# Kernel optimization log

Hardware: AMD Instinct MI355X
Metric: run time of the kernel (lower is better)

The kernel has to match this reference:

```python
import jax, jax.numpy as jnp
import numpy as np


def setup_inputs() -> dict:
    key = jax.random.key(0)
    ks = jax.random.split(key, 7)
    S, B, I, H = 512, 64, 1024, 1024
    s = 1.0 / np.sqrt(H)  # torch Linear default init scale
    return {
        "x": jax.random.normal(ks[0], (S, B, I), dtype=jnp.float32),
        "h0": jax.random.normal(ks[1], (B, H), dtype=jnp.float32),
        "c0": jax.random.normal(ks[2], (B, H), dtype=jnp.float32),
        "W_ih": jax.random.normal(ks[3], (4 * H, I), dtype=jnp.float32) * s,
        "b_ih": jax.random.normal(ks[4], (4 * H,), dtype=jnp.float32) * s,
        "W_hh": jax.random.normal(ks[5], (4 * H, H), dtype=jnp.float32) * s,
        "b_hh": jax.random.normal(ks[6], (4 * H,), dtype=jnp.float32) * s,
    }


def reference(x, h0, c0, W_ih, b_ih, W_hh, b_hh):
    # x: [S, B, I]; LSTM scan over time. Precompute input projections in one
    # big GEMM (mathematically identical to per-step linear_ih).
    H = h0.shape[-1]
    gates_x = jnp.einsum('sbi,gi->sbg', x, W_ih) + b_ih + b_hh  # [S, B, 4H]

    def step(carry, gx):
        h, c = carry
        gates = gx + h @ W_hh.T  # [B, 4H]
        i_g, f_g, g_g, o_g = jnp.split(gates, 4, axis=-1)
        i_g = jax.nn.sigmoid(i_g)
        f_g = jax.nn.sigmoid(f_g)
        g_g = jnp.tanh(g_g)
        o_g = jax.nn.sigmoid(o_g)
        c_new = f_g * c + i_g * g_g
        h_new = o_g * jnp.tanh(c_new)
        return (h_new, c_new), h_new

    (h_last, c_last), output = jax.lax.scan(step, (h0, c0), gates_x)
    return output, (h_last, c_last)
```

## Files before the change

kernel.cpp:

```cpp
#include <hip/hip_runtime.h>
#include <hip/hip_bf16.h>
#include <math.h>


#define S_LEN 512
#define BATCH 64
#define IDIM 1024
#define HDIM 1024
#define GDIM 4096
#define MAGIC 0x1337BEEFu
#define HSLOT (BATCH * HDIM)
#define NRING 4
#define RB 16

typedef __bf16 bf16x8 __attribute__((ext_vector_type(8)));
typedef float f32x4 __attribute__((ext_vector_type(4)));

__device__ inline ushort f2b(float f) {
    union { float f; unsigned u; } v; v.f = f;
    unsigned u = v.u;
    unsigned r = (u + 0x7fffu + ((u >> 16) & 1u)) >> 16;
    return (ushort)r;
}
__device__ inline float b2f(ushort u) {
    union { unsigned u; float f; } v; v.u = ((unsigned)u) << 16;
    return v.f;
}
__device__ inline float sigmoidf_(float x) { return 1.f / (1.f + __expf(-x)); }
__device__ inline float tanhf_(float x) {
    return 1.f - 2.f / (__expf(2.f * x) + 1.f);
}

__global__ __launch_bounds__(256) void f2b_kernel(ushort* __restrict__ dst,
                                                  const float* __restrict__ src, int n) {
    int i = (blockIdx.x * 256 + threadIdx.x) * 4;
    if (i < n) {
        float4 v = *(const float4*)(src + i);
        ushort4 o;
        o.x = f2b(v.x); o.y = f2b(v.y); o.z = f2b(v.z); o.w = f2b(v.w);
        *(ushort4*)(dst + i) = o;
    }
}

__global__ __launch_bounds__(256) void bias_kernel(float* __restrict__ bias,
                                                   const float* __restrict__ b_ih,
                                                   const float* __restrict__ b_hh) {
    int i = blockIdx.x * 256 + threadIdx.x;
    if (i < GDIM) bias[i] = b_ih[i] + b_hh[i];
}

#define LDSS 72
__global__ __launch_bounds__(256) void gemm_bt_kernel(const ushort* __restrict__ A,
                                                      const ushort* __restrict__ B,
                                                      ushort* __restrict__ C,
                                                      int M, int N, int K) {
    __shared__ __align__(16) ushort As[128 * LDSS];
    __shared__ __align__(16) ushort Bs[128 * LDSS];
    const int tid = threadIdx.x;
    const int lane = tid & 63;
    const int wave = tid >> 6;
    const int l15 = lane & 15;
    const int quad = lane >> 4;
    const int bn = blockIdx.x;
    const int bm = blockIdx.y;
    const int wrow = (wave & 1) * 64;
    const int wcol = (wave >> 1) * 64;

    f32x4 acc[4][4] = {};

    for (int kt = 0; kt < K; kt += 64) {
        #pragma unroll
        for (int i = 0; i < 4; i++) {
            int chunk = tid + i * 256;
            int r = chunk >> 3;
            int c8 = (chunk & 7) * 8;
            *(uint4*)&As[r * LDSS + c8] =
                *(const uint4*)&A[(size_t)(bm * 128 + r) * K + kt + c8];
            *(uint4*)&Bs[r * LDSS + c8] =
                *(const uint4*)&B[(size_t)(bn * 128 + r) * K + kt + c8];
        }
        __syncthreads();
        #pragma unroll
        for (int kc = 0; kc < 2; kc++) {
            const int ko = kc * 32 + quad * 8;
            bf16x8 af[4], bf[4];
            #pragma unroll
            for (int m = 0; m < 4; m++)
                af[m] = *(const bf16x8*)&As[(wrow + m * 16 + l15) * LDSS + ko];
            #pragma unroll
            for (int n = 0; n < 4; n++)
                bf[n] = *(const bf16x8*)&Bs[(wcol + n * 16 + l15) * LDSS + ko];
            #pragma unroll
            for (int m = 0; m < 4; m++)
                #pragma unroll
                for (int n = 0; n < 4; n++)
                    acc[m][n] = __builtin_amdgcn_mfma_f32_16x16x32_bf16(af[m], bf[n], acc[m][n], 0, 0, 0);
        }
        __syncthreads();
    }
    const int col0 = bn * 128 + wcol;
    const int row0 = bm * 128 + wrow;
    #pragma unroll
    for (int m = 0; m < 4; m++) {
        #pragma unroll
        for (int n = 0; n < 4; n++) {
            int col = col0 + n * 16 + l15;
            int rbase = row0 + m * 16 + quad * 4;
            #pragma unroll
            for (int r = 0; r < 4; r++)
                C[(size_t)(rbase + r) * N + col] = f2b(acc[m][n][r]);
        }
    }
}

#define HS2 1032
#define GS_BS 17
#define GS_GATE (16 * GS_BS)
#define GS_KH (4 * GS_GATE)

__global__ __launch_bounds__(512, 2) void lstm_persistent(
    const ushort* __restrict__ gx,
    ushort* __restrict__ hring,
    const ushort* __restrict__ Whh,
    const float* __restrict__ bias,
    const float* __restrict__ c0,
    float* __restrict__ out,
    unsigned* __restrict__ flags)
{
    __shared__ __align__(16) ushort Hs[RB * HS2];
    __shared__ float Gs[2 * GS_KH];

    const int tid = threadIdx.x;
    const int lane = tid & 63;
    const int wv = tid >> 6;
    const int gate = wv & 3;
    const int kh = wv >> 2;
    const int l15 = lane & 15;
    const int quad = lane >> 4;
    const int bid = blockIdx.x;
    const int ring = bid >> 6;
    const int blk = bid & 63;

    bf16x8 wf[16];
    {
        const ushort* wrow = Whh + ((size_t)(gate * 1024 + blk * 16 + l15)) * 1024
                           + kh * 512 + quad * 8;
        #pragma unroll
        for (int ks = 0; ks < 16; ks++)
            wf[ks] = *(const bf16x8*)(wrow + ks * 32);
    }

    const bool pw = (tid < 128);
    const int pb = tid >> 3;
    const int pj = (tid * 2) & 15;
    const int gb = ring * RB + pb;
    const int pcol = blk * 16 + pj;
    float2 creg = {0.f, 0.f};
    if (pw) creg = *(const float2*)&c0[(size_t)gb * HDIM + pcol];
    float bsum[4][2];
    #pragma unroll
    for (int g = 0; g < 4; g++) {
        bsum[g][0] = bias[g * 1024 + pcol];
        bsum[g][1] = bias[g * 1024 + pcol + 1];
    }
    const size_t gx_tb = (size_t)gb * GDIM + blk * 16 + pj;

    #pragma unroll 1
    for (int s = 0; s < S_LEN; s++) {
        const ushort* hsrc = hring + (size_t)s * HSLOT + (size_t)ring * RB * HDIM;

        ushort2 gxr[4] = {};
        if (pw) {
            const ushort* gxs = gx + (size_t)s * BATCH * GDIM + gx_tb;
            #pragma unroll
            for (int g = 0; g < 4; g++)
                gxr[g] = *(const ushort2*)(gxs + g * 1024);
        }

        if (s > 0) {
            if (wv == 0) {
                const unsigned* fl = flags + ((size_t)s * NRING + ring) * 64;
                while (true) {
                    unsigned v = __hip_atomic_load(&fl[lane], __ATOMIC_RELAXED,
                                                   __HIP_MEMORY_SCOPE_AGENT);
                    if (__ballot(v != MAGIC) == 0ull) break;
                    __builtin_amdgcn_s_sleep(2);
                }
            }
            __syncthreads();
        }

        {
            const unsigned long long* h64 = (const unsigned long long*)hsrc;
            unsigned long long hr[8];
            #pragma unroll
            for (int c = 0; c < 8; c++)
                hr[c] = __hip_atomic_load(&h64[c * 512 + tid], __ATOMIC_RELAXED,
                                          __HIP_MEMORY_SCOPE_AGENT);
            #pragma unroll
            for (int c = 0; c < 8; c++) {
                int u = c * 512 + tid;
                int row = u >> 8;
                int col = (u & 255) * 4;
                *(unsigned long long*)&Hs[row * HS2 + col] = hr[c];
            }
        }
        __syncthreads();

        f32x4 acc = {0.f, 0.f, 0.f, 0.f};
        const int arow = l15 * HS2 + kh * 512 + quad * 8;
        #pragma unroll
        for (int ks = 0; ks < 16; ks++) {
            bf16x8 a = *(const bf16x8*)&Hs[arow + ks * 32];
            acc = __builtin_amdgcn_mfma_f32_16x16x32_bf16(a, wf[ks], acc, 0, 0, 0);
        }

        #pragma unroll
        for (int r = 0; r < 4; r++)
            Gs[kh * GS_KH + gate * GS_GATE + (quad * 4 + r) * GS_BS + l15] = acc[r];
        __syncthreads();

        float hv[2], cv[2];
        if (pw) {
            #pragma unroll
            for (int u = 0; u < 2; u++) {
                float cold = u ? creg.y : creg.x;
                int gsb = pb * GS_BS + pj + u;
                float g0 = Gs[0 * GS_GATE + gsb] + Gs[GS_KH + 0 * GS_GATE + gsb] + bsum[0][u] + b2f(u ? gxr[0].y : gxr[0].x);
                float g1 = Gs[1 * GS_GATE + gsb] + Gs[GS_KH + 1 * GS_GATE + gsb] + bsum[1][u] + b2f(u ? gxr[1].y : gxr[1].x);
                float g2 = Gs[2 * GS_GATE + gsb] + Gs[GS_KH + 2 * GS_GATE + gsb] + bsum[2][u] + b2f(u ? gxr[2].y : gxr[2].x);
                float g3 = Gs[3 * GS_GATE + gsb] + Gs[GS_KH + 3 * GS_GATE + gsb] + bsum[3][u] + b2f(u ? gxr[3].y : gxr[3].x);
                float ig = sigmoidf_(g0);
                float fg = sigmoidf_(g1);
                float gg = tanhf_(g2);
                float og = sigmoidf_(g3);
                float cn = fg * cold + ig * gg;
                float hn = og * tanhf_(cn);
                cv[u] = cn; hv[u] = hn;
            }
            creg.x = cv[0]; creg.y = cv[1];

            if (s < S_LEN - 1) {
                ushort* hdst = hring + (size_t)(s + 1) * HSLOT;
                unsigned hword = (unsigned)f2b(hv[0]) | ((unsigned)f2b(hv[1]) << 16);
                __hip_atomic_store((unsigned*)&hdst[(size_t)gb * HDIM + pcol], hword,
                                   __ATOMIC_RELAXED, __HIP_MEMORY_SCOPE_AGENT);
            }
        }

        __syncthreads();
        if (tid == 0 && s < S_LEN - 1) {
            asm volatile("s_waitcnt vmcnt(0)" ::: "memory");
            __hip_atomic_store(&flags[((size_t)(s + 1) * NRING + ring) * 64 + blk],
                               MAGIC, __ATOMIC_RELAXED, __HIP_MEMORY_SCOPE_AGENT);
        }

        if (pw) {
            float2 ho; ho.x = hv[0]; ho.y = hv[1];
            *(float2*)&out[(size_t)s * BATCH * HDIM + (size_t)gb * HDIM + pcol] = ho;
            if (s == S_LEN - 1) {
                float* tail = out + (size_t)S_LEN * BATCH * HDIM;
                *(float2*)&tail[(size_t)gb * HDIM + pcol] = ho;
                float2 co; co.x = cv[0]; co.y = cv[1];
                *(float2*)&tail[BATCH * HDIM + (size_t)gb * HDIM + pcol] = co;
            }
        }
    }
}

extern "C" void kernel_launch(void* const* d_in, const int* in_sizes, int n_in,
                              void* d_out, int out_size, void* d_ws, size_t ws_size,
                              hipStream_t stream) {
    const float* x    = (const float*)d_in[0];
    const float* h0   = (const float*)d_in[1];
    const float* c0   = (const float*)d_in[2];
    const float* W_ih = (const float*)d_in[3];
    const float* b_ih = (const float*)d_in[4];
    const float* W_hh = (const float*)d_in[5];
    const float* b_hh = (const float*)d_in[6];
    float* out = (float*)d_out;

    const size_t n_x  = (size_t)S_LEN * BATCH * IDIM;
    const size_t n_w  = (size_t)GDIM * IDIM;
    const size_t o_xb    = 0;
    const size_t o_gx    = o_xb + n_x * 2;
    const size_t o_wih   = o_gx + (size_t)S_LEN * BATCH * GDIM * 2;
    const size_t o_whh   = o_wih + n_w * 2;
    const size_t o_bias  = o_whh + n_w * 2;
    const size_t o_flags = o_bias + GDIM * 4;
    const size_t flags_bytes = (size_t)(S_LEN + 1) * NRING * 64 * 4;
    const size_t total  = o_flags + flags_bytes;
    if (ws_size < total) return;

    char* ws = (char*)d_ws;
    ushort* xb   = (ushort*)(ws + o_xb);
    ushort* hring = xb;
    ushort* gx   = (ushort*)(ws + o_gx);
    ushort* wihb = (ushort*)(ws + o_wih);
    ushort* whhb = (ushort*)(ws + o_whh);
    float*  bias = (float*)(ws + o_bias);
    unsigned* flags = (unsigned*)(ws + o_flags);

    f2b_kernel<<<(int)(n_x / 1024), 256, 0, stream>>>(xb, x, (int)n_x);
    f2b_kernel<<<(int)(n_w / 1024), 256, 0, stream>>>(wihb, W_ih, (int)n_w);
    f2b_kernel<<<(int)(n_w / 1024), 256, 0, stream>>>(whhb, W_hh, (int)n_w);
    bias_kernel<<<GDIM / 256, 256, 0, stream>>>(bias, b_ih, b_hh);
    hipMemsetAsync(flags, 0, flags_bytes, stream);

    {
        dim3 grid(GDIM / 128, (S_LEN * BATCH) / 128);
        gemm_bt_kernel<<<grid, 256, 0, stream>>>(xb, wihb, gx, S_LEN * BATCH, IDIM == 0 ? 0 : GDIM, IDIM);
    }

    f2b_kernel<<<(BATCH * HDIM) / 1024, 256, 0, stream>>>(hring, h0, BATCH * HDIM);

    {
        const ushort* gx_c = gx;
        const ushort* whh_c = whhb;
        const float* bias_c = bias;
        void* args[] = { (void*)&gx_c, (void*)&hring, (void*)&whh_c,
                         (void*)&bias_c, (void*)&c0, (void*)&out, (void*)&flags };
        hipLaunchCooperativeKernel((const void*)lstm_persistent, dim3(NRING * 64), dim3(512),
                                   args, 0, stream);
    }
}
```

Baseline: 2.328 ms.

## Pin LSTM batch rings to XCDs so sync stays in local L2

The persistent LSTM is repartitioned into 8 batch rings of 8 rows, with 32 blocks per ring each owning 32 hidden columns (two MFMA column groups). At startup each block reads its XCC_ID and claims a slot, so every ring lives entirely on one XCD. When that placement succeeds, flag polling, h writes and h reads use plain or workgroup-scope accesses that stay in the local L2 instead of agent-scope coherent traffic. The aim is to cut cross-XCD synchronisation latency per timestep. The cost is a startup grid barrier and a fallback path, and correctness relies on the assumption that same-XCD L2 coherence holds for these non-atomic accesses.

```diff
diff --git a/kernel.cpp b/kernel.cpp
--- a/kernel.cpp
+++ b/kernel.cpp
@@ -10,8 +10,10 @@
 #define GDIM 4096
 #define MAGIC 0x1337BEEFu
 #define HSLOT (BATCH * HDIM)
-#define NRING 4
-#define RB 16
+#define NRING 8
+#define RB 8
+#define NBLK 32
+#define CPB 32
 
 typedef __bf16 bf16x8 __attribute__((ext_vector_type(8)));
 typedef float f32x4 __attribute__((ext_vector_type(4)));
@@ -114,9 +116,7 @@
 }
 
 #define HS2 1032
-#define GS_BS 17
-#define GS_GATE (16 * GS_BS)
-#define GS_KH (4 * GS_GATE)
+#define GS_CS 33
 
 __global__ __launch_bounds__(512, 2) void lstm_persistent(
     const ushort* __restrict__ gx,
@@ -125,10 +125,12 @@
     const float* __restrict__ bias,
     const float* __restrict__ c0,
     float* __restrict__ out,
-    unsigned* __restrict__ flags)
+    unsigned* __restrict__ flags,
+    unsigned* __restrict__ claim)
 {
-    __shared__ __align__(16) ushort Hs[RB * HS2];
-    __shared__ float Gs[2 * GS_KH];
+    __shared__ __align__(16) ushort Hs[16 * HS2];
+    __shared__ float Gs[2 * 4 * 16 * GS_CS];
+    __shared__ int sh_ring, sh_pos, sh_ok;
 
     const int tid = threadIdx.x;
     const int lane = tid & 63;
@@ -138,23 +140,51 @@
     const int l15 = lane & 15;
     const int quad = lane >> 4;
     const int bid = blockIdx.x;
-    const int ring = bid >> 6;
-    const int blk = bid & 63;
-
-    bf16x8 wf[16];
+
+    if (tid == 0) {
+        unsigned xcd;
+        asm volatile("s_getreg_b32 %0, hwreg(HW_REG_XCC_ID)" : "=s"(xcd));
+        xcd &= 7;
+        int p = (int)__hip_atomic_fetch_add(&claim[xcd], 1u, __ATOMIC_RELAXED,
+                                            __HIP_MEMORY_SCOPE_AGENT);
+        __hip_atomic_fetch_add(&claim[8], 1u, __ATOMIC_RELEASE,
+                               __HIP_MEMORY_SCOPE_AGENT);
+        while (__hip_atomic_load(&claim[8], __ATOMIC_RELAXED,
+                                 __HIP_MEMORY_SCOPE_AGENT) < NRING * NBLK)
+            __builtin_amdgcn_s_sleep(8);
+        int ok = 1;
+        #pragma unroll
+        for (int i = 0; i < 8; i++)
+            ok &= (__hip_atomic_load(&claim[i], __ATOMIC_RELAXED,
+                                     __HIP_MEMORY_SCOPE_AGENT) == NBLK);
+        sh_ring = ok ? (int)xcd : (bid & 7);
+        sh_pos  = ok ? p : (bid >> 3);
+        sh_ok = ok;
+    }
+    for (int i = tid; i < 8 * HS2; i += 512) Hs[8 * HS2 + i] = 0;
+    __syncthreads();
+    const int ring = sh_ring;
+    const int pos = sh_pos;
+    const bool l2ok = (sh_ok != 0);
+
+    bf16x8 wf[2][16];
     {
-        const ushort* wrow = Whh + ((size_t)(gate * 1024 + blk * 16 + l15)) * 1024
-                           + kh * 512 + quad * 8;
-        #pragma unroll
-        for (int ks = 0; ks < 16; ks++)
-            wf[ks] = *(const bf16x8*)(wrow + ks * 32);
+        #pragma unroll
+        for (int cg = 0; cg < 2; cg++) {
+            const ushort* wrow = Whh
+                + ((size_t)(gate * 1024 + pos * CPB + cg * 16 + l15)) * 1024
+                + kh * 512 + quad * 8;
+            #pragma unroll
+            for (int ks = 0; ks < 16; ks++)
+                wf[cg][ks] = *(const bf16x8*)(wrow + ks * 32);
+        }
     }
 
     const bool pw = (tid < 128);
-    const int pb = tid >> 3;
-    const int pj = (tid * 2) & 15;
+    const int pb = tid >> 4;
+    const int pj = (tid & 15) * 2;
     const int gb = ring * RB + pb;
-    const int pcol = blk * 16 + pj;
+    const int pcol = pos * CPB + pj;
     float2 creg = {0.f, 0.f};
     if (pw) creg = *(const float2*)&c0[(size_t)gb * HDIM + pcol];
     float bsum[4][2];
@@ -163,7 +193,7 @@
         bsum[g][0] = bias[g * 1024 + pcol];
         bsum[g][1] = bias[g * 1024 + pcol + 1];
     }
-    const size_t gx_tb = (size_t)gb * GDIM + blk * 16 + pj;
+    const size_t gx_tb = (size_t)gb * GDIM + pcol;
 
     #pragma unroll 1
     for (int s = 0; s < S_LEN; s++) {
@@ -179,26 +209,51 @@
 
         if (s > 0) {
             if (wv == 0) {
-                const unsigned* fl = flags + ((size_t)s * NRING + ring) * 64;
-                while (true) {
-                    unsigned v = __hip_atomic_load(&fl[lane], __ATOMIC_RELAXED,
-                                                   __HIP_MEMORY_SCOPE_AGENT);
-                    if (__ballot(v != MAGIC) == 0ull) break;
-                    __builtin_amdgcn_s_sleep(2);
+                unsigned* fp = flags + ((size_t)s * NRING + ring) * NBLK + (lane & 31);
+                if (l2ok) {
+                    while (true) {
+                        unsigned exp = MAGIC;
+                        if (lane < 32)
+                            __hip_atomic_compare_exchange_strong(
+                                fp, &exp, MAGIC, __ATOMIC_RELAXED,
+                                __ATOMIC_RELAXED, __HIP_MEMORY_SCOPE_WORKGROUP);
+                        if (__ballot(exp != MAGIC) == 0ull) break;
+                        __builtin_amdgcn_s_sleep(1);
+                    }
+                } else {
+                    while (true) {
+                        unsigned v = __hip_atomic_load(fp, __ATOMIC_RELAXED,
+                                                       __HIP_MEMORY_SCOPE_AGENT);
+                        if (__ballot(v != MAGIC) == 0ull) break;
+                        __builtin_amdgcn_s_sleep(2);
+                    }
                 }
             }
             __syncthreads();
         }
 
-        {
+        if (l2ok) {
+            const uint4* h128 = (const uint4*)hsrc;
+            uint4 hr[2];
+            #pragma unroll
+            for (int c = 0; c < 2; c++)
+                hr[c] = h128[c * 512 + tid];
+            #pragma unroll
+            for (int c = 0; c < 2; c++) {
+                int u = c * 512 + tid;
+                int row = u >> 7;
+                int col = (u & 127) * 8;
+                *(uint4*)&Hs[row * HS2 + col] = hr[c];
+            }
+        } else {
             const unsigned long long* h64 = (const unsigned long long*)hsrc;
-            unsigned long long hr[8];
-            #pragma unroll
-            for (int c = 0; c < 8; c++)
+            unsigned long long hr[4];
+            #pragma unroll
+            for (int c = 0; c < 4; c++)
                 hr[c] = __hip_atomic_load(&h64[c * 512 + tid], __ATOMIC_RELAXED,
                                           __HIP_MEMORY_SCOPE_AGENT);
             #pragma unroll
-            for (int c = 0; c < 8; c++) {
+            for (int c = 0; c < 4; c++) {
                 int u = c * 512 + tid;
                 int row = u >> 8;
                 int col = (u & 255) * 4;
@@ -207,17 +262,20 @@
         }
         __syncthreads();
 
-        f32x4 acc = {0.f, 0.f, 0.f, 0.f};
+        f32x4 acc[2] = {};
         const int arow = l15 * HS2 + kh * 512 + quad * 8;
         #pragma unroll
         for (int ks = 0; ks < 16; ks++) {
             bf16x8 a = *(const bf16x8*)&Hs[arow + ks * 32];
-            acc = __builtin_amdgcn_mfma_f32_16x16x32_bf16(a, wf[ks], acc, 0, 0, 0);
-        }
-
-        #pragma unroll
-        for (int r = 0; r < 4; r++)
-            Gs[kh * GS_KH + gate * GS_GATE + (quad * 4 + r) * GS_BS + l15] = acc[r];
+            acc[0] = __builtin_amdgcn_mfma_f32_16x16x32_bf16(a, wf[0][ks], acc[0], 0, 0, 0);
+            acc[1] = __builtin_amdgcn_mfma_f32_16x16x32_bf16(a, wf[1][ks], acc[1], 0, 0, 0);
+        }
+
+        #pragma unroll
+        for (int cg = 0; cg < 2; cg++)
+            #pragma unroll
+            for (int r = 0; r < 4; r++)
+                Gs[((kh * 4 + gate) * 16 + quad * 4 + r) * GS_CS + cg * 16 + l15] = acc[cg][r];
         __syncthreads();
 
         float hv[2], cv[2];
@@ -225,11 +283,18 @@
             #pragma unroll
             for (int u = 0; u < 2; u++) {
                 float cold = u ? creg.y : creg.x;
-                int gsb = pb * GS_BS + pj + u;
-                float g0 = Gs[0 * GS_GATE + gsb] + Gs[GS_KH + 0 * GS_GATE + gsb] + bsum[0][u] + b2f(u ? gxr[0].y : gxr[0].x);
-                float g1 = Gs[1 * GS_GATE + gsb] + Gs[GS_KH + 1 * GS_GATE + gsb] + bsum[1][u] + b2f(u ? gxr[1].y : gxr[1].x);
-                float g2 = Gs[2 * GS_GATE + gsb] + Gs[GS_KH + 2 * GS_GATE + gsb] + bsum[2][u] + b2f(u ? gxr[2].y : gxr[2].x);
-                float g3 = Gs[3 * GS_GATE + gsb] + Gs[GS_KH + 3 * GS_GATE + gsb] + bsum[3][u] + b2f(u ? gxr[3].y : gxr[3].x);
+                float g0 = Gs[((0 * 4 + 0) * 16 + pb) * GS_CS + pj + u]
+                         + Gs[((1 * 4 + 0) * 16 + pb) * GS_CS + pj + u]
+                         + bsum[0][u] + b2f(u ? gxr[0].y : gxr[0].x);
+                float g1 = Gs[((0 * 4 + 1) * 16 + pb) * GS_CS + pj + u]
+                         + Gs[((1 * 4 + 1) * 16 + pb) * GS_CS + pj + u]
+                         + bsum[1][u] + b2f(u ? gxr[1].y : gxr[1].x);
+                float g2 = Gs[((0 * 4 + 2) * 16 + pb) * GS_CS + pj + u]
+                         + Gs[((1 * 4 + 2) * 16 + pb) * GS_CS + pj + u]
+                         + bsum[2][u] + b2f(u ? gxr[2].y : gxr[2].x);
+                float g3 = Gs[((0 * 4 + 3) * 16 + pb) * GS_CS + pj + u]
+                         + Gs[((1 * 4 + 3) * 16 + pb) * GS_CS + pj + u]
+                         + bsum[3][u] + b2f(u ? gxr[3].y : gxr[3].x);
                 float ig = sigmoidf_(g0);
                 float fg = sigmoidf_(g1);
                 float gg = tanhf_(g2);
@@ -241,18 +306,28 @@
             creg.x = cv[0]; creg.y = cv[1];
 
             if (s < S_LEN - 1) {
-                ushort* hdst = hring + (size_t)(s + 1) * HSLOT;
+                unsigned* hd = (unsigned*)(hring + (size_t)(s + 1) * HSLOT
+                                           + (size_t)gb * HDIM + pcol);
                 unsigned hword = (unsigned)f2b(hv[0]) | ((unsigned)f2b(hv[1]) << 16);
-                __hip_atomic_store((unsigned*)&hdst[(size_t)gb * HDIM + pcol], hword,
-                                   __ATOMIC_RELAXED, __HIP_MEMORY_SCOPE_AGENT);
+                if (l2ok) {
+                    *hd = hword;
+                } else {
+                    __hip_atomic_store(hd, hword, __ATOMIC_RELAXED,
+                                       __HIP_MEMORY_SCOPE_AGENT);
+                }
             }
         }
 
         __syncthreads();
         if (tid == 0 && s < S_LEN - 1) {
             asm volatile("s_waitcnt vmcnt(0)" ::: "memory");
-            __hip_atomic_store(&flags[((size_t)(s + 1) * NRING + ring) * 64 + blk],
-                               MAGIC, __ATOMIC_RELAXED, __HIP_MEMORY_SCOPE_AGENT);
+            unsigned* fd = flags + ((size_t)(s + 1) * NRING + ring) * NBLK + pos;
+            if (l2ok) {
+                *fd = MAGIC;
+            } else {
+                __hip_atomic_store(fd, MAGIC, __ATOMIC_RELAXED,
+                                   __HIP_MEMORY_SCOPE_AGENT);
+            }
         }
 
         if (pw) {
@@ -288,8 +363,10 @@
     const size_t o_whh   = o_wih + n_w * 2;
     const size_t o_bias  = o_whh + n_w * 2;
     const size_t o_flags = o_bias + GDIM * 4;
-    const size_t flags_bytes = (size_t)(S_LEN + 1) * NRING * 64 * 4;
-    const size_t total  = o_flags + flags_bytes;
+    const size_t flags_bytes = (size_t)(S_LEN + 1) * NRING * NBLK * 4;
+    const size_t o_claim = o_flags + flags_bytes;
+    const size_t claim_bytes = 64;
+    const size_t total  = o_claim + claim_bytes;
     if (ws_size < total) return;
 
     char* ws = (char*)d_ws;
@@ -300,16 +377,17 @@
     ushort* whhb = (ushort*)(ws + o_whh);
     float*  bias = (float*)(ws + o_bias);
     unsigned* flags = (unsigned*)(ws + o_flags);
+    unsigned* claim = (unsigned*)(ws + o_claim);
 
     f2b_kernel<<<(int)(n_x / 1024), 256, 0, stream>>>(xb, x, (int)n_x);
     f2b_kernel<<<(int)(n_w / 1024), 256, 0, stream>>>(wihb, W_ih, (int)n_w);
     f2b_kernel<<<(int)(n_w / 1024), 256, 0, stream>>>(whhb, W_hh, (int)n_w);
     bias_kernel<<<GDIM / 256, 256, 0, stream>>>(bias, b_ih, b_hh);
-    hipMemsetAsync(flags, 0, flags_bytes, stream);
+    hipMemsetAsync(flags, 0, flags_bytes + claim_bytes, stream);
 
     {
         dim3 grid(GDIM / 128, (S_LEN * BATCH) / 128);
-        gemm_bt_kernel<<<grid, 256, 0, stream>>>(xb, wihb, gx, S_LEN * BATCH, IDIM == 0 ? 0 : GDIM, IDIM);
+        gemm_bt_kernel<<<grid, 256, 0, stream>>>(xb, wihb, gx, S_LEN * BATCH, GDIM, IDIM);
     }
 
     f2b_kernel<<<(BATCH * HDIM) / 1024, 256, 0, stream>>>(hring, h0, BATCH * HDIM);
@@ -319,8 +397,9 @@
         const ushort* whh_c = whhb;
         const float* bias_c = bias;
         void* args[] = { (void*)&gx_c, (void*)&hring, (void*)&whh_c,
-                         (void*)&bias_c, (void*)&c0, (void*)&out, (void*)&flags };
-        hipLaunchCooperativeKernel((const void*)lstm_persistent, dim3(NRING * 64), dim3(512),
+                         (void*)&bias_c, (void*)&c0, (void*)&out, (void*)&flags,
+                         (void*)&claim };
+        hipLaunchCooperativeKernel((const void*)lstm_persistent, dim3(NRING * NBLK), dim3(512),
                                    args, 0, stream);
     }
 }
```

Result: slower. 2.723 ms (+17.0%).
